# Optimization experiments

Hardware: AMD Instinct MI355X
Metric: run time of the kernel (lower is better)

## Reference

```python
import jax, jax.numpy as jnp
import numpy as np

NC = 4        # num_components
HEADS = 24
DH = 64
D = HEADS * DH  # 1536
EPS = 1e-8


def setup_inputs() -> dict:
    key = jax.random.key(0)
    ks = jax.random.split(key, 7)
    btc, S, E = 4, 4096, 154
    w = lambda k: jax.random.normal(k, (D, D), jnp.float32) * 0.02
    return {
        "hidden_states": jax.random.normal(ks[0], (btc, S, D), jnp.float32),
        "encoder_hidden_states": jax.random.normal(ks[1], (btc, E, D), jnp.float32),
        "temperature": jnp.ones((1,), jnp.float32),
        "Wq": w(ks[2]),
        "Wk": w(ks[3]),
        "Wv": w(ks[4]),
        "Wo": w(ks[5]),
        "bo": jnp.zeros((D,), jnp.float32),
        "pad_length": 154,
    }


def reference(hidden_states, encoder_hidden_states, temperature, Wq, Wk, Wv, Wo, bo, pad_length):
    btc, S, d = hidden_states.shape          # batch*components, latent seq, hidden
    E = encoder_hidden_states.shape[1]       # encoder seq (== pad_length)
    b = btc // NC
    scale = DH ** -0.5
    residual = hidden_states

    def heads(x, L):  # [btc, L, D] -> [btc, H, L, dh]
        return x.reshape(btc, L, HEADS, DH).transpose(0, 2, 1, 3)

    q = heads(hidden_states @ Wq.T, S)
    k = heads(encoder_hidden_states @ Wk.T, E)
    v = heads(encoder_hidden_states @ Wv.T, E)

    # pad tokens are zeros projected through the same k/v weights (no bias -> zeros)
    pad_h = jnp.zeros((btc, pad_length, d), hidden_states.dtype)
    k_pad = heads(pad_h @ Wk.T, pad_length)
    v_pad = heads(pad_h @ Wv.T, pad_length)

    scores = jnp.einsum('bhsd,bhed->bhse', q, k) / (temperature[0] + EPS)
    scores_pad = jnp.einsum('bhsd,bhpd->bhsp', q, k_pad) * scale

    # cross-component softmax over dim 0
    scores = scores.reshape(NC, b, HEADS, S, E)
    scores_pad = scores_pad.reshape(NC, b, HEADS, S, pad_length)
    w = jax.nn.softmax(scores, axis=0)
    w_pad = jax.nn.softmax(scores_pad, axis=0) * (NC / pad_length) * (1.0 - w)

    weights = jnp.concatenate(
        [w.reshape(btc, HEADS, S, E), w_pad.reshape(btc, HEADS, S, pad_length)],
        axis=-1)                              # [btc, H, S, E+pad]
    v_cat = jnp.concatenate([v, v_pad], axis=2)  # [btc, H, E+pad, dh]

    out = jnp.einsum('bhse,bhed->bhsd', weights, v_cat)
    out = out.transpose(0, 2, 1, 3).reshape(btc, S, d)
    out = out @ Wo.T + bo
    return out + residual
```

## Files before the change

### kernel.cpp

```cpp
#include <hip/hip_runtime.h>

typedef __attribute__((ext_vector_type(8))) short short8;
typedef __attribute__((ext_vector_type(4))) float f32x4;
typedef __attribute__((ext_vector_type(4))) unsigned short us4;
typedef __attribute__((ext_vector_type(4))) float float4v;

#define GLB_PTR(p) ((const __attribute__((address_space(1))) void*)(p))
#define LDS_PTR(p) ((__attribute__((address_space(3))) void*)(p))

__device__ __forceinline__ unsigned short f2bf(float f) {
  unsigned int u = __float_as_uint(f);
  u += 0x7FFF + ((u >> 16) & 1);
  return (unsigned short)(u >> 16);
}

__global__ void cvt_kernel(const float* __restrict__ in, unsigned short* __restrict__ out, int n4) {
  int i = blockIdx.x * blockDim.x + threadIdx.x;
  int stride = gridDim.x * blockDim.x;
  for (; i < n4; i += stride) {
    float4v v = *(const float4v*)(in + (size_t)i * 4);
    us4 o;
    o[0] = f2bf(v[0]); o[1] = f2bf(v[1]); o[2] = f2bf(v[2]); o[3] = f2bf(v[3]);
    *(us4*)(out + (size_t)i * 4) = o;
  }
}

__global__ void cvt4_kernel(const float* __restrict__ w0, const float* __restrict__ w1,
                            const float* __restrict__ w2, const float* __restrict__ w3,
                            unsigned short* __restrict__ o0, unsigned short* __restrict__ o1,
                            unsigned short* __restrict__ o2, unsigned short* __restrict__ o3,
                            int n4) {
  const float* in = blockIdx.y == 0 ? w0 : blockIdx.y == 1 ? w1 : blockIdx.y == 2 ? w2 : w3;
  unsigned short* out = blockIdx.y == 0 ? o0 : blockIdx.y == 1 ? o1 : blockIdx.y == 2 ? o2 : o3;
  int i = blockIdx.x * blockDim.x + threadIdx.x;
  int stride = gridDim.x * blockDim.x;
  for (; i < n4; i += stride) {
    float4v v = *(const float4v*)(in + (size_t)i * 4);
    us4 o;
    o[0] = f2bf(v[0]); o[1] = f2bf(v[1]); o[2] = f2bf(v[2]); o[3] = f2bf(v[3]);
    *(us4*)(out + (size_t)i * 4) = o;
  }
}

template<int MODE>
__global__ __launch_bounds__(256, 2) void gemm_big(
    const unsigned short* __restrict__ A,
    const unsigned short* __restrict__ B,
    unsigned short* __restrict__ Cb,
    float* __restrict__ Cf,
    const float* __restrict__ bias,
    const float* __restrict__ resid) {
  constexpr int K = 1536, N = 1536, BK = 32, NKT = K / BK;
  __shared__ unsigned short As[2][256 * 32];
  __shared__ unsigned short Bs[2][128 * 32];

  const int bid = blockIdx.x;
  const int xcd = bid & 7, idx = bid >> 3;
  const int m0 = (xcd * 8 + idx / 12) * 256;
  const int n0 = (idx % 12) * 128;

  const int t = threadIdx.x;
  const int w = t >> 6, l = t & 63, lr = l & 15, lg = l >> 4;
  const int wr = w >> 1, wc = w & 1;
  const int ga = lg ^ (lr & 3);

  const int srow = t >> 2;
  const int sg = (t & 3) ^ (srow & 3);
  const unsigned short* aSrc = A + (size_t)(m0 + srow) * K + sg * 8;
  const unsigned short* bSrc = B + (size_t)(n0 + srow) * K + sg * 8;

  f32x4 acc[8][4] = {};

  auto stage = [&](int buf, int k0) {
    unsigned short* AsW = &As[buf][0] + w * 512;
    unsigned short* BsW = &Bs[buf][0] + w * 512;
#pragma unroll
    for (int i = 0; i < 4; ++i)
      __builtin_amdgcn_global_load_lds(GLB_PTR(aSrc + (size_t)(i * 64) * K + k0), LDS_PTR(AsW + i * 2048), 16, 0, 0);
#pragma unroll
    for (int i = 0; i < 2; ++i)
      __builtin_amdgcn_global_load_lds(GLB_PTR(bSrc + (size_t)(i * 64) * K + k0), LDS_PTR(BsW + i * 2048), 16, 0, 0);
  };

  auto compute = [&](const unsigned short* Asb, const unsigned short* Bsb) {
    short8 af[8], bfv[4];
#pragma unroll
    for (int i = 0; i < 8; ++i)
      af[i] = *(const short8*)(Asb + (wr * 128 + i * 16 + lr) * 32 + ga * 8);
#pragma unroll
    for (int j = 0; j < 4; ++j)
      bfv[j] = *(const short8*)(Bsb + (wc * 64 + j * 16 + lr) * 32 + ga * 8);
#pragma unroll
    for (int i = 0; i < 8; ++i)
#pragma unroll
      for (int j = 0; j < 4; ++j)
        acc[i][j] = __builtin_amdgcn_mfma_f32_16x16x32_bf16(af[i], bfv[j], acc[i][j], 0, 0, 0);
  };

  stage(0, 0);
  __syncthreads();
  for (int kt = 0; kt < NKT; kt += 2) {
    if (kt + 1 < NKT) stage(1, (kt + 1) * BK);
    compute(&As[0][0], &Bs[0][0]);
    __syncthreads();
    if (kt + 2 < NKT) stage(0, (kt + 2) * BK);
    compute(&As[1][0], &Bs[1][0]);
    __syncthreads();
  }

#pragma unroll
  for (int i = 0; i < 8; ++i) {
    const int rb = m0 + wr * 128 + i * 16 + lg * 4;
#pragma unroll
    for (int j = 0; j < 4; ++j) {
      const int col = n0 + wc * 64 + j * 16 + lr;
#pragma unroll
      for (int r = 0; r < 4; ++r) {
        size_t o = (size_t)(rb + r) * N + col;
        if (MODE == 0) Cb[o] = f2bf(acc[i][j][r]);
        else           Cf[o] = acc[i][j][r] + bias[col] + resid[o];
      }
    }
  }
}

__global__ __launch_bounds__(256) void gemm_kv(
    const unsigned short* __restrict__ A,
    const unsigned short* __restrict__ Bk,
    const unsigned short* __restrict__ Bv,
    unsigned short* __restrict__ Ck,
    unsigned short* __restrict__ Cv) {
  constexpr int K = 1536, N = 1536, Mc = 615;
  __shared__ unsigned short As[128 * 32];
  __shared__ unsigned short Bs[128 * 32];
  const unsigned short* B = blockIdx.y < 12 ? Bk : Bv;
  unsigned short* C = blockIdx.y < 12 ? Ck : Cv;
  const int m0 = blockIdx.x * 128, n0 = (blockIdx.y % 12) * 128;
  const int t = threadIdx.x;
  const int w = t >> 6, l = t & 63, lr = l & 15, lg = l >> 4;
  const int wr = w >> 1, wc = w & 1;
  const int srow = t >> 2, scol = (t & 3) * 8;

  f32x4 acc[4][4] = {};
  unsigned short* AsW = As + w * 512;
  unsigned short* BsW = Bs + w * 512;
  long ar0 = m0 + srow;       if (ar0 > Mc) ar0 = Mc;
  long ar1 = m0 + srow + 64;  if (ar1 > Mc) ar1 = Mc;

  for (int k0 = 0; k0 < K; k0 += 32) {
    __builtin_amdgcn_global_load_lds(GLB_PTR(A + ar0 * (long)K + k0 + scol), LDS_PTR(AsW),        16, 0, 0);
    __builtin_amdgcn_global_load_lds(GLB_PTR(A + ar1 * (long)K + k0 + scol), LDS_PTR(AsW + 2048), 16, 0, 0);
    __builtin_amdgcn_global_load_lds(GLB_PTR(B + (long)(n0 + srow) * K + k0 + scol),      LDS_PTR(BsW),        16, 0, 0);
    __builtin_amdgcn_global_load_lds(GLB_PTR(B + (long)(n0 + srow + 64) * K + k0 + scol), LDS_PTR(BsW + 2048), 16, 0, 0);
    __syncthreads();

    short8 af[4], bfv[4];
#pragma unroll
    for (int i = 0; i < 4; ++i) {
      af[i]  = *(const short8*)(As + (wr * 64 + i * 16 + lr) * 32 + lg * 8);
      bfv[i] = *(const short8*)(Bs + (wc * 64 + i * 16 + lr) * 32 + lg * 8);
    }
#pragma unroll
    for (int i = 0; i < 4; ++i)
#pragma unroll
      for (int j = 0; j < 4; ++j)
        acc[i][j] = __builtin_amdgcn_mfma_f32_16x16x32_bf16(af[i], bfv[j], acc[i][j], 0, 0, 0);
    __syncthreads();
  }

#pragma unroll
  for (int i = 0; i < 4; ++i) {
    int rb = m0 + wr * 64 + i * 16 + lg * 4;
#pragma unroll
    for (int j = 0; j < 4; ++j) {
      int col = n0 + wc * 64 + j * 16 + lr;
#pragma unroll
      for (int r = 0; r < 4; ++r)
        C[(long)(rb + r) * N + col] = f2bf(acc[i][j][r]);
    }
  }
}

__global__ void vtrans(const unsigned short* __restrict__ Vb, unsigned short* __restrict__ Vt) {
  int c = blockIdx.x / 24, h = blockIdx.x % 24;
  for (int idx = threadIdx.x; idx < 64 * 160; idx += blockDim.x) {
    int d = idx & 63, e = idx >> 6;
    unsigned short v = 0;
    if (e < 154) v = Vb[(long)(c * 154 + e) * 1536 + h * 64 + d];
    Vt[((long)((c * 24 + h) * 64 + d)) * 160 + e] = v;
  }
}

__global__ __launch_bounds__(256) void attn_kernel(
    const unsigned short* __restrict__ Qb,
    const unsigned short* __restrict__ Kb,
    const unsigned short* __restrict__ Vt,
    const float* __restrict__ temp,
    unsigned short* __restrict__ Ob) {
  __shared__ unsigned short P[4][4][16][160];
  const int h = blockIdx.y, sb = blockIdx.x;
  const int t = threadIdx.x, w = t >> 6, l = t & 63, lr = l & 15, lg = l >> 4;
  const int s0 = sb * 64 + w * 16;
  const float sc = 1.0f / (temp[0] + 1e-8f);

  short8 qf[4][2];
#pragma unroll
  for (int c = 0; c < 4; ++c)
#pragma unroll
    for (int kt = 0; kt < 2; ++kt)
      qf[c][kt] = *(const short8*)(Qb + (long)(c * 4096 + s0 + lr) * 1536 + h * 64 + kt * 32 + lg * 8);

  for (int et = 0; et < 10; ++et) {
    f32x4 sa[4] = {};
#pragma unroll
    for (int c = 0; c < 4; ++c)
#pragma unroll
      for (int kt = 0; kt < 2; ++kt) {
        short8 kf = *(const short8*)(Kb + (long)(c * 154 + et * 16 + lr) * 1536 + h * 64 + kt * 32 + lg * 8);
        sa[c] = __builtin_amdgcn_mfma_f32_16x16x32_bf16(kf, qf[c][kt], sa[c], 0, 0, 0);
      }
    float wv[4][4];
#pragma unroll
    for (int r = 0; r < 4; ++r) {
      float x0 = sa[0][r] * sc, x1 = sa[1][r] * sc, x2 = sa[2][r] * sc, x3 = sa[3][r] * sc;
      float m = fmaxf(fmaxf(x0, x1), fmaxf(x2, x3));
      float e0 = __expf(x0 - m), e1 = __expf(x1 - m), e2 = __expf(x2 - m), e3 = __expf(x3 - m);
      float inv = 1.0f / (e0 + e1 + e2 + e3);
      wv[0][r] = e0 * inv; wv[1][r] = e1 * inv; wv[2][r] = e2 * inv; wv[3][r] = e3 * inv;
    }
#pragma unroll
    for (int c = 0; c < 4; ++c) {
      us4 pk;
      pk[0] = f2bf(wv[c][0]); pk[1] = f2bf(wv[c][1]); pk[2] = f2bf(wv[c][2]); pk[3] = f2bf(wv[c][3]);
      *(us4*)&P[w][c][lr][et * 16 + lg * 4] = pk;
    }
  }
  __syncthreads();

  f32x4 o[4][4] = {};
#pragma unroll
  for (int c = 0; c < 4; ++c)
    for (int ks = 0; ks < 5; ++ks) {
      short8 pf = *(const short8*)&P[w][c][lr][ks * 32 + lg * 8];
#pragma unroll
      for (int nt = 0; nt < 4; ++nt) {
        short8 vf = *(const short8*)(Vt + (long)((c * 24 + h) * 64 + nt * 16 + lr) * 160 + ks * 32 + lg * 8);
        o[c][nt] = __builtin_amdgcn_mfma_f32_16x16x32_bf16(pf, vf, o[c][nt], 0, 0, 0);
      }
    }

#pragma unroll
  for (int c = 0; c < 4; ++c)
#pragma unroll
    for (int nt = 0; nt < 4; ++nt)
#pragma unroll
      for (int r = 0; r < 4; ++r)
        Ob[(long)(c * 4096 + s0 + lg * 4 + r) * 1536 + h * 64 + nt * 16 + lr] = f2bf(o[c][nt][r]);
}

extern "C" void kernel_launch(void* const* d_in, const int* in_sizes, int n_in,
                              void* d_out, int out_size, void* d_ws, size_t ws_size,
                              hipStream_t stream) {
  (void)in_sizes; (void)n_in; (void)out_size; (void)ws_size;
  const float* HS  = (const float*)d_in[0];
  const float* EHS = (const float*)d_in[1];
  const float* TMP = (const float*)d_in[2];
  const float* Wq  = (const float*)d_in[3];
  const float* Wk  = (const float*)d_in[4];
  const float* Wv  = (const float*)d_in[5];
  const float* Wo  = (const float*)d_in[6];
  const float* bo  = (const float*)d_in[7];

  char* ws = (char*)d_ws;
  size_t off = 0;
  unsigned short* HSb  = (unsigned short*)(ws + off); off += (size_t)16384 * 1536 * 2;
  unsigned short* Ob   = HSb;
  unsigned short* EHSb = (unsigned short*)(ws + off); off += (size_t)616 * 1536 * 2;
  unsigned short* Wqb  = (unsigned short*)(ws + off); off += (size_t)1536 * 1536 * 2;
  unsigned short* Wkb  = (unsigned short*)(ws + off); off += (size_t)1536 * 1536 * 2;
  unsigned short* Wvb  = (unsigned short*)(ws + off); off += (size_t)1536 * 1536 * 2;
  unsigned short* Wob  = (unsigned short*)(ws + off); off += (size_t)1536 * 1536 * 2;
  unsigned short* Kb   = (unsigned short*)(ws + off); off += (size_t)640 * 1536 * 2;
  unsigned short* Vb   = (unsigned short*)(ws + off); off += (size_t)640 * 1536 * 2;
  unsigned short* Vt   = (unsigned short*)(ws + off); off += (size_t)4 * 24 * 64 * 160 * 2;
  unsigned short* Qb   = (unsigned short*)d_out;

  cvt_kernel<<<2048, 256, 0, stream>>>(HS,  HSb,  16384 * 1536 / 4);
  cvt_kernel<<<512,  256, 0, stream>>>(EHS, EHSb, 616 * 1536 / 4);
  cvt4_kernel<<<dim3(576, 4), 256, 0, stream>>>(Wq, Wk, Wv, Wo, Wqb, Wkb, Wvb, Wob, 1536 * 1536 / 4);

  gemm_big<0><<<768, 256, 0, stream>>>(HSb, Wqb, Qb, nullptr, nullptr, nullptr);
  gemm_kv<<<dim3(5, 24), 256, 0, stream>>>(EHSb, Wkb, Wvb, Kb, Vb);

  vtrans<<<96, 256, 0, stream>>>(Vb, Vt);

  attn_kernel<<<dim3(64, 24), 256, 0, stream>>>(Qb, Kb, Vt, TMP, Ob);

  gemm_big<1><<<768, 256, 0, stream>>>(Ob, Wob, nullptr, (float*)d_out, bo, HS);
}
```

Baseline: 420.2 us.

## Triple-buffer GEMM LDS staging with explicit vmcnt waits and MFMA priority

Moves the large bf16 GEMM from a double-buffered LDS loop to a three-stage ring buffer, so three K-tiles of loads are in flight. Each iteration waits on vmcnt for only the oldest tile, reads fragments into registers, then barriers and reissues loads into the freed slot before running the MFMAs. The MFMAs run at raised wave priority. This is meant to hide global-to-LDS latency better. In exchange, LDS use grows by half, which could limit the two-blocks-per-CU occupancy, and correctness relies on hand-counted vmcnt values.

```diff
diff --git a/kernel.cpp b/kernel.cpp
--- a/kernel.cpp
+++ b/kernel.cpp
@@ -51,8 +51,8 @@
     const float* __restrict__ bias,
     const float* __restrict__ resid) {
   constexpr int K = 1536, N = 1536, BK = 32, NKT = K / BK;
-  __shared__ unsigned short As[2][256 * 32];
-  __shared__ unsigned short Bs[2][128 * 32];
+  __shared__ unsigned short As[3][256 * 32];
+  __shared__ unsigned short Bs[3][128 * 32];
 
   const int bid = blockIdx.x;
   const int xcd = bid & 7, idx = bid >> 3;
@@ -71,7 +71,8 @@
 
   f32x4 acc[8][4] = {};
 
-  auto stage = [&](int buf, int k0) {
+  auto stage = [&](int buf, int kt) {
+    const int k0 = kt * BK;
     unsigned short* AsW = &As[buf][0] + w * 512;
     unsigned short* BsW = &Bs[buf][0] + w * 512;
 #pragma unroll
@@ -82,14 +83,18 @@
       __builtin_amdgcn_global_load_lds(GLB_PTR(bSrc + (size_t)(i * 64) * K + k0), LDS_PTR(BsW + i * 2048), 16, 0, 0);
   };
 
-  auto compute = [&](const unsigned short* Asb, const unsigned short* Bsb) {
-    short8 af[8], bfv[4];
+  auto loadfrags = [&](int buf, short8* af, short8* bfv) {
+    const unsigned short* Asb = &As[buf][0];
+    const unsigned short* Bsb = &Bs[buf][0];
 #pragma unroll
     for (int i = 0; i < 8; ++i)
       af[i] = *(const short8*)(Asb + (wr * 128 + i * 16 + lr) * 32 + ga * 8);
 #pragma unroll
     for (int j = 0; j < 4; ++j)
       bfv[j] = *(const short8*)(Bsb + (wc * 64 + j * 16 + lr) * 32 + ga * 8);
+  };
+
+  auto mfma_all = [&](short8* af, short8* bfv) {
 #pragma unroll
     for (int i = 0; i < 8; ++i)
 #pragma unroll
@@ -97,15 +102,36 @@
         acc[i][j] = __builtin_amdgcn_mfma_f32_16x16x32_bf16(af[i], bfv[j], acc[i][j], 0, 0, 0);
   };
 
-  stage(0, 0);
-  __syncthreads();
-  for (int kt = 0; kt < NKT; kt += 2) {
-    if (kt + 1 < NKT) stage(1, (kt + 1) * BK);
-    compute(&As[0][0], &Bs[0][0]);
-    __syncthreads();
-    if (kt + 2 < NKT) stage(0, (kt + 2) * BK);
-    compute(&As[1][0], &Bs[1][0]);
-    __syncthreads();
+  stage(0, 0); stage(1, 1); stage(2, 2);
+
+  int cur = 0;
+  for (int kt = 0; kt < NKT - 3; ++kt) {
+    asm volatile("s_waitcnt vmcnt(12)" ::: "memory");
+    __builtin_amdgcn_s_barrier();
+    __builtin_amdgcn_sched_barrier(0);
+    short8 af[8], bfv[4];
+    loadfrags(cur, af, bfv);
+    asm volatile("s_waitcnt lgkmcnt(0)" ::: "memory");
+    __builtin_amdgcn_sched_barrier(0);
+    __builtin_amdgcn_s_barrier();
+    __builtin_amdgcn_sched_barrier(0);
+    stage(cur, kt + 3);
+    __builtin_amdgcn_s_setprio(1);
+    mfma_all(af, bfv);
+    __builtin_amdgcn_s_setprio(0);
+    cur = cur + 1; if (cur == 3) cur = 0;
+  }
+#pragma unroll
+  for (int j = 0; j < 3; ++j) {
+    if (j == 0)      asm volatile("s_waitcnt vmcnt(12)" ::: "memory");
+    else if (j == 1) asm volatile("s_waitcnt vmcnt(6)" ::: "memory");
+    else             asm volatile("s_waitcnt vmcnt(0)" ::: "memory");
+    __builtin_amdgcn_s_barrier();
+    __builtin_amdgcn_sched_barrier(0);
+    short8 af[8], bfv[4];
+    loadfrags(cur, af, bfv);
+    mfma_all(af, bfv);
+    cur = cur + 1; if (cur == 3) cur = 0;
   }
 
 #pragma unroll
```

Result: faster. 404.1 us (-3.8%).

## Restructure big GEMM into 256x256 tiles with 8 waves and staggered quarter-tile pipeline

Applied to the files above, without the earlier changes.

The Q-projection and output-projection GEMM moves from 256x128 tiles with 4 waves and BK=32 to 256x256 tiles with 8 waves and BK=64. Loads are issued in quarter-tile pieces interleaved with MFMA quadrants, using explicit vmcnt/lgkmcnt waits, barriers, sched_barrier and setprio. The aim is to raise arithmetic intensity per LDS byte and overlap global-to-LDS traffic with compute. It doubles LDS to 128KB per block, which limits occupancy, and relies on fragile hand-tuned wait counts.

```diff
diff --git a/kernel.cpp b/kernel.cpp
--- a/kernel.cpp
+++ b/kernel.cpp
@@ -42,70 +42,116 @@
   }
 }
 
+template<int H, int G>
+__device__ __forceinline__ void mfq(f32x4 (&acc)[8][4], const short8* a, const short8* b) {
+#pragma unroll
+  for (int i2 = 0; i2 < 4; ++i2)
+#pragma unroll
+    for (int j2 = 0; j2 < 2; ++j2)
+#pragma unroll
+      for (int kk = 0; kk < 2; ++kk)
+        acc[H * 4 + i2][G * 2 + j2] = __builtin_amdgcn_mfma_f32_16x16x32_bf16(
+            a[i2 * 2 + kk], b[j2 * 2 + kk], acc[H * 4 + i2][G * 2 + j2], 0, 0, 0);
+}
+
 template<int MODE>
-__global__ __launch_bounds__(256, 2) void gemm_big(
+__global__ __launch_bounds__(512, 2) void gemm_big(
     const unsigned short* __restrict__ A,
     const unsigned short* __restrict__ B,
     unsigned short* __restrict__ Cb,
     float* __restrict__ Cf,
     const float* __restrict__ bias,
     const float* __restrict__ resid) {
-  constexpr int K = 1536, N = 1536, BK = 32, NKT = K / BK;
-  __shared__ unsigned short As[2][256 * 32];
-  __shared__ unsigned short Bs[2][128 * 32];
+  constexpr int K = 1536, N = 1536, BK = 64, NKT = K / BK;
+  __shared__ unsigned short As[2][256 * 64];
+  __shared__ unsigned short Bs[2][256 * 64];
 
   const int bid = blockIdx.x;
   const int xcd = bid & 7, idx = bid >> 3;
-  const int m0 = (xcd * 8 + idx / 12) * 256;
-  const int n0 = (idx % 12) * 128;
+  const int m0 = (xcd * 8 + idx / 6) * 256;
+  const int n0 = (idx % 6) * 256;
 
   const int t = threadIdx.x;
   const int w = t >> 6, l = t & 63, lr = l & 15, lg = l >> 4;
-  const int wr = w >> 1, wc = w & 1;
-  const int ga = lg ^ (lr & 3);
-
-  const int srow = t >> 2;
-  const int sg = (t & 3) ^ (srow & 3);
-  const unsigned short* aSrc = A + (size_t)(m0 + srow) * K + sg * 8;
-  const unsigned short* bSrc = B + (size_t)(n0 + srow) * K + sg * 8;
+  const int wr = w >> 2, wc = w & 3;
+
+  const int srow = w * 8 + (l >> 3);
+  const int sgi  = (l & 7) ^ ((l >> 3) & 7);
+  const int rdsw = lr & 7;
 
   f32x4 acc[8][4] = {};
 
-  auto stage = [&](int buf, int k0) {
-    unsigned short* AsW = &As[buf][0] + w * 512;
-    unsigned short* BsW = &Bs[buf][0] + w * 512;
-#pragma unroll
-    for (int i = 0; i < 4; ++i)
-      __builtin_amdgcn_global_load_lds(GLB_PTR(aSrc + (size_t)(i * 64) * K + k0), LDS_PTR(AsW + i * 2048), 16, 0, 0);
-#pragma unroll
-    for (int i = 0; i < 2; ++i)
-      __builtin_amdgcn_global_load_lds(GLB_PTR(bSrc + (size_t)(i * 64) * K + k0), LDS_PTR(BsW + i * 2048), 16, 0, 0);
+  auto stageA = [&](int d, int q, int kt) {
+    if (kt >= NKT) kt -= NKT;
+    const unsigned short* src = A + (size_t)(m0 + q * 64 + srow) * K + kt * 64 + sgi * 8;
+#pragma unroll
+    for (int j = 0; j < 2; ++j)
+      __builtin_amdgcn_global_load_lds(GLB_PTR(src + (size_t)j * 128 * K),
+          LDS_PTR(&As[d][(q * 64 + j * 128 + w * 8) * 64]), 16, 0, 0);
   };
-
-  auto compute = [&](const unsigned short* Asb, const unsigned short* Bsb) {
-    short8 af[8], bfv[4];
-#pragma unroll
-    for (int i = 0; i < 8; ++i)
-      af[i] = *(const short8*)(Asb + (wr * 128 + i * 16 + lr) * 32 + ga * 8);
-#pragma unroll
-    for (int j = 0; j < 4; ++j)
-      bfv[j] = *(const short8*)(Bsb + (wc * 64 + j * 16 + lr) * 32 + ga * 8);
-#pragma unroll
-    for (int i = 0; i < 8; ++i)
-#pragma unroll
-      for (int j = 0; j < 4; ++j)
-        acc[i][j] = __builtin_amdgcn_mfma_f32_16x16x32_bf16(af[i], bfv[j], acc[i][j], 0, 0, 0);
+  auto stageB = [&](int d, int g, int kt) {
+    if (kt >= NKT) kt -= NKT;
+    const int rb = g * 32 + (w >> 1) * 64 + (w & 1) * 16;
+    const unsigned short* src = B + (size_t)(n0 + rb + (l >> 3)) * K + kt * 64 + sgi * 8;
+#pragma unroll
+    for (int j = 0; j < 2; ++j)
+      __builtin_amdgcn_global_load_lds(GLB_PTR(src + (size_t)j * 8 * K),
+          LDS_PTR(&Bs[d][(rb + j * 8) * 64]), 16, 0, 0);
   };
-
-  stage(0, 0);
-  __syncthreads();
-  for (int kt = 0; kt < NKT; kt += 2) {
-    if (kt + 1 < NKT) stage(1, (kt + 1) * BK);
-    compute(&As[0][0], &Bs[0][0]);
-    __syncthreads();
-    if (kt + 2 < NKT) stage(0, (kt + 2) * BK);
-    compute(&As[1][0], &Bs[1][0]);
-    __syncthreads();
+  auto readA = [&](int d, int h, short8* a) {
+#pragma unroll
+    for (int i2 = 0; i2 < 4; ++i2)
+#pragma unroll
+      for (int kk = 0; kk < 2; ++kk) {
+        const int row = wr * 128 + (h * 4 + i2) * 16 + lr;
+        const int gi = (kk * 4 + lg) ^ rdsw;
+        a[i2 * 2 + kk] = *(const short8*)(&As[d][row * 64 + gi * 8]);
+      }
+  };
+  auto readB = [&](int d, int g, short8* b) {
+#pragma unroll
+    for (int j2 = 0; j2 < 2; ++j2)
+#pragma unroll
+      for (int kk = 0; kk < 2; ++kk) {
+        const int row = wc * 64 + (g * 2 + j2) * 16 + lr;
+        const int gi = (kk * 4 + lg) ^ rdsw;
+        b[j2 * 2 + kk] = *(const short8*)(&Bs[d][row * 64 + gi * 8]);
+      }
+  };
+
+  short8 aCur[8], b0[4], b1[4];
+
+  stageA(0, 0, 0); stageB(0, 0, 0); stageB(0, 1, 0); stageA(0, 1, 0);
+  stageA(1, 0, 1); stageB(1, 0, 1); stageB(1, 1, 1);
+
+  int d = 0;
+  for (int kt = 0; kt < NKT; ++kt, d ^= 1) {
+    asm volatile("s_waitcnt vmcnt(10)" ::: "memory");
+    __builtin_amdgcn_s_barrier();
+    __builtin_amdgcn_sched_barrier(0);
+    readA(d, 0, aCur); readB(d, 0, b0);
+    stageA(d ^ 1, 1, kt + 1);
+    asm volatile("s_waitcnt lgkmcnt(0)" ::: "memory");
+    __builtin_amdgcn_sched_barrier(0);
+    __builtin_amdgcn_s_setprio(1); mfq<0, 0>(acc, aCur, b0); __builtin_amdgcn_s_setprio(0);
+    asm volatile("s_waitcnt vmcnt(10)" ::: "memory");
+    __builtin_amdgcn_s_barrier();
+    __builtin_amdgcn_sched_barrier(0);
+    readB(d, 1, b1);
+    stageA(d, 0, kt + 2);
+    asm volatile("s_waitcnt lgkmcnt(0)" ::: "memory");
+    __builtin_amdgcn_sched_barrier(0);
+    __builtin_amdgcn_s_setprio(1); mfq<0, 1>(acc, aCur, b1); __builtin_amdgcn_s_setprio(0);
+    asm volatile("s_waitcnt vmcnt(10)" ::: "memory");
+    __builtin_amdgcn_s_barrier();
+    __builtin_amdgcn_sched_barrier(0);
+    readA(d, 1, aCur);
+    stageB(d, 0, kt + 2);
+    asm volatile("s_waitcnt lgkmcnt(0)" ::: "memory");
+    __builtin_amdgcn_sched_barrier(0);
+    __builtin_amdgcn_s_setprio(1); mfq<1, 1>(acc, aCur, b1); __builtin_amdgcn_s_setprio(0);
+    stageB(d, 1, kt + 2);
+    __builtin_amdgcn_s_setprio(1); mfq<1, 0>(acc, aCur, b0); __builtin_amdgcn_s_setprio(0);
   }
 
 #pragma unroll
@@ -289,12 +335,12 @@
   cvt_kernel<<<512,  256, 0, stream>>>(EHS, EHSb, 616 * 1536 / 4);
   cvt4_kernel<<<dim3(576, 4), 256, 0, stream>>>(Wq, Wk, Wv, Wo, Wqb, Wkb, Wvb, Wob, 1536 * 1536 / 4);
 
-  gemm_big<0><<<768, 256, 0, stream>>>(HSb, Wqb, Qb, nullptr, nullptr, nullptr);
+  gemm_big<0><<<384, 512, 0, stream>>>(HSb, Wqb, Qb, nullptr, nullptr, nullptr);
   gemm_kv<<<dim3(5, 24), 256, 0, stream>>>(EHSb, Wkb, Wvb, Kb, Vb);
 
   vtrans<<<96, 256, 0, stream>>>(Vb, Vt);
 
   attn_kernel<<<dim3(64, 24), 256, 0, stream>>>(Qb, Kb, Vt, TMP, Ob);
 
-  gemm_big<1><<<768, 256, 0, stream>>>(Ob, Wob, nullptr, (float*)d_out, bo, HS);
-}
+  gemm_big<1><<<384, 512, 0, stream>>>(Ob, Wob, nullptr, (float*)d_out, bo, HS);
+}
```

Result: no change. 413.4 us (-1.6%).
